# Optimization experiments

Measured on AMD Instinct MI355X. Metric: run time of the kernel, lower is better.

Reference implementation:

```python
import jax, jax.numpy as jnp
import numpy as np

INV_148 = 1.0 / 1.48  # scaling to align grids with flat-top gaussian


def _trilinear_sample(grid, pts):
    # grid: [C, D, H, W]; pts: [N, 3] in (x,y,z)=(W,H,D) normalized coords, align_corners=True,
    # padding_mode='zeros' (out-of-bounds corners contribute 0). Returns [C, N].
    C, D, H, W = grid.shape
    fx = (pts[:, 0] + 1.0) * 0.5 * (W - 1)
    fy = (pts[:, 1] + 1.0) * 0.5 * (H - 1)
    fz = (pts[:, 2] + 1.0) * 0.5 * (D - 1)
    x0 = jnp.floor(fx).astype(jnp.int32)
    y0 = jnp.floor(fy).astype(jnp.int32)
    z0 = jnp.floor(fz).astype(jnp.int32)
    wx, wy, wz = fx - x0, fy - y0, fz - z0
    out = jnp.zeros((C, pts.shape[0]), dtype=grid.dtype)
    for dz in (0, 1):
        for dy in (0, 1):
            for dx in (0, 1):
                xi, yi, zi = x0 + dx, y0 + dy, z0 + dz
                w = (wx if dx else 1.0 - wx) * (wy if dy else 1.0 - wy) * (wz if dz else 1.0 - wz)
                valid = ((xi >= 0) & (xi < W) & (yi >= 0) & (yi < H) & (zi >= 0) & (zi < D))
                v = grid[:, jnp.clip(zi, 0, D - 1), jnp.clip(yi, 0, H - 1), jnp.clip(xi, 0, W - 1)]
                out = out + v * (w * valid)
    return out


def setup_inputs() -> dict:
    key = jax.random.key(0)
    ks = jax.random.split(key, 10)
    G, Fch, Dg, N, NPL, OUT = 32, 2, 64, 524288, 64, 1
    in_dim = G * Fch
    x = jax.random.uniform(ks[0], (N, 3), minval=-1.0, maxval=1.0, dtype=jnp.float32)
    grid_scales = jax.random.uniform(ks[1], (G, 3), minval=1.5, maxval=2.5, dtype=jnp.float32)
    grid_translations = jax.random.uniform(ks[2], (G, 3), minval=-1.0, maxval=1.0, dtype=jnp.float32) * (grid_scales - 1.0)
    feature_grids = jax.random.uniform(ks[3], (G, Fch, Dg, Dg, Dg), minval=-0.001, maxval=0.001, dtype=jnp.float32)
    W0 = jax.random.normal(ks[4], (NPL, in_dim), dtype=jnp.float32) * (1.0 / np.sqrt(in_dim))
    b0 = jnp.zeros((NPL,), dtype=jnp.float32)
    W1 = jax.random.normal(ks[5], (NPL, NPL), dtype=jnp.float32) * (1.0 / np.sqrt(NPL))
    b1 = jnp.zeros((NPL,), dtype=jnp.float32)
    W2 = jax.random.normal(ks[6], (OUT, NPL), dtype=jnp.float32) * (1.0 / np.sqrt(NPL))
    b2 = jnp.zeros((OUT,), dtype=jnp.float32)
    return {"x": x, "grid_scales": grid_scales, "grid_translations": grid_translations,
            "feature_grids": feature_grids, "W0": W0, "b0": b0, "W1": W1, "b1": b1, "W2": W2, "b2": b2}


def reference(x, grid_scales, grid_translations, feature_grids, W0, b0, W1, b1, W2, b2):
    G = feature_grids.shape[0]
    N = x.shape[0]
    # transform(): per-grid affine (diag scale + translation), then * 1/1.48 -> [G, N, 3]
    local = (x[None, :, :] * grid_scales[:, None, :] + grid_translations[:, None, :]) * INV_148
    # forward detaches grid coords before grid_sample
    local = jax.lax.stop_gradient(local)
    feats = jax.vmap(_trilinear_sample)(feature_grids, local)  # [G, F, N]
    h = feats.reshape(G * feats.shape[1], N).T  # [N, G*F]
    h = jax.nn.relu(h @ W0.T + b0)
    h = jax.nn.relu(h @ W1.T + b1)
    return h @ W2.T + b2  # [N, n_outputs]
```

## Files before the change

kernel.cpp:

```cpp
#include <hip/hip_runtime.h>
#include <hip/hip_fp16.h>

#define NG    32
#define DG    64
#define NPL   64
#define CPD2  16
#define NC2   4096
#define NCELL 512
#define HPAD  4
#define BS    512
#define TV    4096
#define HS    68

typedef _Float16 half8 __attribute__((ext_vector_type(8)));
typedef float    floatx4 __attribute__((ext_vector_type(4)));

__global__ void pack_grids_kernel(const float* __restrict__ fg,
                                  uint4* __restrict__ pg, int total4) {
    int idx = blockIdx.x * blockDim.x + threadIdx.x;
    if (idx >= total4) return;
    int g  = idx >> 16;
    int v4 = (idx & 65535) << 2;
    const float* base = fg + ((size_t)g << 19);
    float4 a = *(const float4*)(base + v4);
    float4 b = *(const float4*)(base + (1 << 18) + v4);
    uint4 o;
    __half2 h;
    h = __floats2half2_rn(a.x, b.x); o.x = *(unsigned*)&h;
    h = __floats2half2_rn(a.y, b.y); o.y = *(unsigned*)&h;
    h = __floats2half2_rn(a.z, b.z); o.z = *(unsigned*)&h;
    h = __floats2half2_rn(a.w, b.w); o.w = *(unsigned*)&h;
    pg[idx] = o;
}

__device__ __forceinline__ int morton16(int cx, int cy, int cz) {
    int m = 0;
    #pragma unroll
    for (int b = 0; b < 4; ++b)
        m |= (((cx >> b) & 1) << (3 * b))
           | (((cy >> b) & 1) << (3 * b + 1))
           | (((cz >> b) & 1) << (3 * b + 2));
    return m;
}
__device__ __forceinline__ int cell_of(float px, float py, float pz) {
    int cx = min(max((int)((px + 1.0f) * (0.5f * CPD2)), 0), CPD2 - 1);
    int cy = min(max((int)((py + 1.0f) * (0.5f * CPD2)), 0), CPD2 - 1);
    int cz = min(max((int)((pz + 1.0f) * (0.5f * CPD2)), 0), CPD2 - 1);
    return morton16(cx, cy, cz);
}

__global__ __launch_bounds__(BS)
void hist_kernel(const float* __restrict__ x, int N, int* __restrict__ ghist) {
    __shared__ int lh[NC2];
    for (int i = threadIdx.x; i < NC2; i += BS) lh[i] = 0;
    __syncthreads();
    int n = blockIdx.x * BS + threadIdx.x;
    if (n < N) atomicAdd(&lh[cell_of(x[3*n], x[3*n+1], x[3*n+2])], 1);
    __syncthreads();
    for (int i = threadIdx.x; i < NC2; i += BS) {
        int c = lh[i];
        if (c) atomicAdd(&ghist[i * HPAD], c);
    }
}

__global__ __launch_bounds__(1024)
void scan_kernel(const int* __restrict__ ghist, int* __restrict__ gcursor,
                 int* __restrict__ cellstart) {
    __shared__ int tsum[1024];
    int t = threadIdx.x;
    int v0 = ghist[(t * 4 + 0) * HPAD];
    int v1 = ghist[(t * 4 + 1) * HPAD];
    int v2 = ghist[(t * 4 + 2) * HPAD];
    int v3 = ghist[(t * 4 + 3) * HPAD];
    tsum[t] = v0 + v1 + v2 + v3;
    __syncthreads();
    #pragma unroll
    for (int off = 1; off < 1024; off <<= 1) {
        int u = (t >= off) ? tsum[t - off] : 0;
        __syncthreads();
        tsum[t] += u;
        __syncthreads();
    }
    int base = (t == 0) ? 0 : tsum[t - 1];
    gcursor[(t*4+0)*HPAD] = base; cellstart[t*4+0] = base; base += v0;
    gcursor[(t*4+1)*HPAD] = base; cellstart[t*4+1] = base; base += v1;
    gcursor[(t*4+2)*HPAD] = base; cellstart[t*4+2] = base; base += v2;
    gcursor[(t*4+3)*HPAD] = base; cellstart[t*4+3] = base;
    if (t == 1023) cellstart[NC2] = tsum[1023];
}

__global__ __launch_bounds__(BS)
void scatter_kernel(const float* __restrict__ x, int N,
                    int* __restrict__ gcursor, float4* __restrict__ sorted,
                    int* __restrict__ nidx) {
    __shared__ int cnt[NC2];
    __shared__ int base[NC2];
    int tid = threadIdx.x;
    for (int i = tid; i < NC2; i += BS) cnt[i] = 0;
    __syncthreads();
    int n = blockIdx.x * BS + tid;
    float px = 0.f, py = 0.f, pz = 0.f;
    int c = 0, r = 0;
    bool act = (n < N);
    if (act) {
        px = x[3*n]; py = x[3*n+1]; pz = x[3*n+2];
        c = cell_of(px, py, pz);
        r = atomicAdd(&cnt[c], 1);
    }
    __syncthreads();
    for (int i = tid; i < NC2; i += BS) {
        int cc = cnt[i];
        base[i] = cc ? atomicAdd(&gcursor[i * HPAD], cc) : 0;
    }
    __syncthreads();
    if (act) {
        int pos = base[c] + r;
        sorted[pos] = make_float4(px, py, pz, 0.0f);
        nidx[pos]   = n;
    }
}

__device__ __forceinline__ float2 h2_to_f2(unsigned u) {
    __half2 h = *reinterpret_cast<__half2*>(&u);
    return __half22float2(h);
}

template<bool FAST>
__device__ __forceinline__ unsigned sample_tile(
    const unsigned* __restrict__ tl,
    float px, float py, float pz,
    float A0, float A1, float A2, float B0, float B1, float B2,
    int ox, int oy, int oz)
{
    float fx = fmaf(px, A0, B0);
    float fy = fmaf(py, A1, B1);
    float fz = fmaf(pz, A2, B2);
    float flx = floorf(fx), fly = floorf(fy), flz = floorf(fz);
    int x0 = (int)flx, y0 = (int)fly, z0 = (int)flz;
    float wx = fx - flx, wy = fy - fly, wz = fz - flz;

    float wxa0, wxa1, wya0, wya1, wza0, wza1;
    if (FAST) {
        wxa0 = 1.0f - wx; wxa1 = wx;
        wya0 = 1.0f - wy; wya1 = wy;
        wza0 = 1.0f - wz; wza1 = wz;
    } else {
        wxa0 = (x0 >= 0  && x0     < DG) ? (1.0f - wx) : 0.0f;
        wxa1 = (x0 >= -1 && x0 + 1 < DG) ? wx          : 0.0f;
        wya0 = (y0 >= 0  && y0     < DG) ? (1.0f - wy) : 0.0f;
        wya1 = (y0 >= -1 && y0 + 1 < DG) ? wy          : 0.0f;
        wza0 = (z0 >= 0  && z0     < DG) ? (1.0f - wz) : 0.0f;
        wza1 = (z0 >= -1 && z0 + 1 < DG) ? wz          : 0.0f;
    }
    int ix0 = min(max(x0     - ox, 0), 15);
    int ix1 = min(max(x0 + 1 - ox, 0), 15);
    int iy0 = (min(max(y0     - oy, 0), 15)) << 4;
    int iy1 = (min(max(y0 + 1 - oy, 0), 15)) << 4;
    int iz0 = (min(max(z0     - oz, 0), 15)) << 8;
    int iz1 = (min(max(z0 + 1 - oz, 0), 15)) << 8;

    float w00 = wya0 * wza0, w10 = wya1 * wza0;
    float w01 = wya0 * wza1, w11 = wya1 * wza1;

    float c0 = 0.0f, c1 = 0.0f;
    float2 v;
    v = h2_to_f2(tl[iz0+iy0+ix0]); c0 = fmaf(wxa0*w00, v.x, c0); c1 = fmaf(wxa0*w00, v.y, c1);
    v = h2_to_f2(tl[iz0+iy0+ix1]); c0 = fmaf(wxa1*w00, v.x, c0); c1 = fmaf(wxa1*w00, v.y, c1);
    v = h2_to_f2(tl[iz0+iy1+ix0]); c0 = fmaf(wxa0*w10, v.x, c0); c1 = fmaf(wxa0*w10, v.y, c1);
    v = h2_to_f2(tl[iz0+iy1+ix1]); c0 = fmaf(wxa1*w10, v.x, c0); c1 = fmaf(wxa1*w10, v.y, c1);
    v = h2_to_f2(tl[iz1+iy0+ix0]); c0 = fmaf(wxa0*w01, v.x, c0); c1 = fmaf(wxa0*w01, v.y, c1);
    v = h2_to_f2(tl[iz1+iy0+ix1]); c0 = fmaf(wxa1*w01, v.x, c0); c1 = fmaf(wxa1*w01, v.y, c1);
    v = h2_to_f2(tl[iz1+iy1+ix0]); c0 = fmaf(wxa0*w11, v.x, c0); c1 = fmaf(wxa0*w11, v.y, c1);
    v = h2_to_f2(tl[iz1+iy1+ix1]); c0 = fmaf(wxa1*w11, v.x, c0); c1 = fmaf(wxa1*w11, v.y, c1);

    __half2 hv = __floats2half2_rn(c0, c1);
    return *reinterpret_cast<unsigned*>(&hv);
}

__global__ __launch_bounds__(BS)
void gather_kernel(const float4* __restrict__ sorted,
                   const int*   __restrict__ cs16,
                   const float* __restrict__ scales,
                   const float* __restrict__ trans,
                   const unsigned* __restrict__ pg,
                   int4* __restrict__ featbuf, int N)
{
    __shared__ float    sA[NG * 3];
    __shared__ float    sB[NG * 3];
    __shared__ int      sO[NG * 3];
    __shared__ int      sCls[NG];
    __shared__ int      sList[NG + 1];
    __shared__ unsigned tile[2][TV];

    const int tid  = threadIdx.x;
    const int bid  = blockIdx.x;
    const int half = bid >> 9;
    const int cell = bid & 511;
    const int c    = ((cell & 7) << 6) + (cell >> 3);

    int s0c = cs16[c * 8];
    int ec  = cs16[c * 8 + 8];
    int cnt = ec - s0c;
    int hsz = (cnt + 1) >> 1;
    int start = s0c + half * hsz;
    int end   = min(ec, start + hsz);
    if (start >= end) return;

    int cx = (c & 1)        | (((c >> 3) & 1) << 1) | (((c >> 6) & 1) << 2);
    int cy = ((c >> 1) & 1) | (((c >> 4) & 1) << 1) | (((c >> 7) & 1) << 2);
    int cz = ((c >> 2) & 1) | (((c >> 5) & 1) << 1) | (((c >> 8) & 1) << 2);

    if (tid < NG * 3) {
        const float k = (1.0f / 1.48f) * 31.5f;
        float A  = scales[tid] * k;
        float Bv = trans[tid] * k + 31.5f;
        sA[tid] = A; sB[tid] = Bv;
        int d  = tid % 3;
        int cc = (d == 0) ? cx : ((d == 1) ? cy : cz);
        int o  = (int)floorf(fmaf((float)cc * 0.25f - 1.0f, A, Bv));
        sO[tid] = min(max(o, 0), 48);
    }
    __syncthreads();
    if (tid < NG) {
        bool skip = false, fast = true;
        #pragma unroll
        for (int d = 0; d < 3; ++d) {
            float A = sA[3 * tid + d], B = sB[3 * tid + d];
            int  cc = (d == 0) ? cx : ((d == 1) ? cy : cz);
            float lo = fmaf((float)cc, 0.25f, -1.0f) - 1e-4f;
            float hi = lo + 0.25f + 2e-4f;
            float fmn = fmaf(lo, A, B);
            float fmx = fmaf(hi, A, B);
            skip = skip || (fmx <= -1.0f) || (fmn >= 64.0f);
            fast = fast && (fmn >= 0.0f) && (fmx <= 63.0f);
        }
        sCls[tid] = skip ? 0 : (fast ? 1 : 2);
    }
    __syncthreads();
    if (tid == 0) {
        int n2 = 0;
        for (int g = 0; g < NG; ++g)
            if (sCls[g]) sList[n2++] = g;
        sList[NG] = n2;
    }
    __syncthreads();
    const int nAct = sList[NG];

    int  ip0 = start + tid,        ip1 = start + BS + tid;
    bool act0 = (ip0 < end),       act1 = (ip1 < end);
    float px0 = 0.f, py0 = 0.f, pz0 = 0.f;
    float px1 = 0.f, py1 = 0.f, pz1 = 0.f;
    if (act0) { float4 q = sorted[ip0]; px0 = q.x; py0 = q.y; pz0 = q.z; }
    if (act1) { float4 q = sorted[ip1]; px1 = q.x; py1 = q.y; pz1 = q.z; }

    if (nAct > 0) {
        int g0 = sList[0];
        int ox = sO[3*g0], oy = sO[3*g0+1], oz = sO[3*g0+2];
        const unsigned* gb = pg + ((size_t)g0 << 18);
        #pragma unroll
        for (int jj = 0; jj < 8; ++jj) {
            int v = tid + (jj << 9);
            tile[0][v] = gb[((oz + (v >> 8)) << 12) + ((oy + ((v >> 4) & 15)) << 6)
                            + ox + (v & 15)];
        }
    }
    __syncthreads();

    unsigned fp0[4], fp1[4];
    unsigned r[8];
    int j = 0;

    #pragma unroll 1
    for (int w = 0; w < 8; ++w) {
        #pragma unroll
        for (int q = 0; q < 4; ++q) {
            int g   = 4 * w + q;
            int cls = sCls[g];
            if (cls == 0) { fp0[q] = 0u; fp1[q] = 0u; continue; }

            const unsigned* tl = &tile[j & 1][0];
            bool more = (j + 1 < nAct);
            if (more) {
                int gn = sList[j + 1];
                int ox = sO[3*gn], oy = sO[3*gn+1], oz = sO[3*gn+2];
                const unsigned* gb = pg + ((size_t)gn << 18);
                #pragma unroll
                for (int jj = 0; jj < 8; ++jj) {
                    int v = tid + (jj << 9);
                    r[jj] = gb[((oz + (v >> 8)) << 12) + ((oy + ((v >> 4) & 15)) << 6)
                               + ox + (v & 15)];
                }
            }

            float A0 = sA[3*g], A1 = sA[3*g+1], A2 = sA[3*g+2];
            float B0 = sB[3*g], B1 = sB[3*g+1], B2 = sB[3*g+2];
            int   ox = sO[3*g], oy = sO[3*g+1], oz = sO[3*g+2];
            if (cls == 1) {
                fp0[q] = act0 ? sample_tile<true >(tl, px0,py0,pz0, A0,A1,A2,B0,B1,B2, ox,oy,oz) : 0u;
                fp1[q] = act1 ? sample_tile<true >(tl, px1,py1,pz1, A0,A1,A2,B0,B1,B2, ox,oy,oz) : 0u;
            } else {
                fp0[q] = act0 ? sample_tile<false>(tl, px0,py0,pz0, A0,A1,A2,B0,B1,B2, ox,oy,oz) : 0u;
                fp1[q] = act1 ? sample_tile<false>(tl, px1,py1,pz1, A0,A1,A2,B0,B1,B2, ox,oy,oz) : 0u;
            }

            if (more) {
                unsigned* td = &tile[(j & 1) ^ 1][0];
                #pragma unroll
                for (int jj = 0; jj < 8; ++jj) td[tid + (jj << 9)] = r[jj];
            }
            __syncthreads();
            ++j;
        }
        const size_t plane = (size_t)w * (size_t)N;
        if (act0) featbuf[plane + ip0] =
            make_int4((int)fp0[0], (int)fp0[1], (int)fp0[2], (int)fp0[3]);
        if (act1) featbuf[plane + ip1] =
            make_int4((int)fp1[0], (int)fp1[1], (int)fp1[2], (int)fp1[3]);
    }
}

#define MBS 256
__global__ __launch_bounds__(MBS)
void mlp_kernel(const int4* __restrict__ featbuf,
                const int* __restrict__ nidx,
                const float* __restrict__ W0, const float* __restrict__ b0,
                const float* __restrict__ W1, const float* __restrict__ b1,
                const float* __restrict__ W2, const float* __restrict__ b2,
                float* __restrict__ out, int N)
{
    __shared__ __align__(16) _Float16 sW0h[NPL * NPL];
    __shared__ __align__(16) _Float16 sW1h[NPL * NPL];
    __shared__ float sb0f[NPL], sb1f[NPL], sW2f[NPL];
    __shared__ __align__(16) _Float16 sH[4][NPL * HS];

    int tid = threadIdx.x;
    for (int i = tid; i < NPL * NPL; i += MBS) {
        sW0h[i] = (_Float16)W0[i];
        sW1h[i] = (_Float16)W1[i];
    }
    if (tid < NPL) { sb0f[tid] = b0[tid]; sb1f[tid] = b1[tid]; sW2f[tid] = W2[tid]; }
    __syncthreads();

    const int wave = tid >> 6;
    const int lane = tid & 63;
    const int l15  = lane & 15;
    const int kg   = lane >> 4;
    const long wbase = (long)blockIdx.x * MBS + wave * 64;
    if (wbase >= N) return;

    half8 B0[4][2], B1[4][2];
    float bias0[4], bias1[4], w2v[4];
    #pragma unroll
    for (int nt = 0; nt < 4; ++nt) {
        int ch = nt * 16 + l15;
        #pragma unroll
        for (int kh = 0; kh < 2; ++kh) {
            int k = kh * 32 + kg * 8;
            B0[nt][kh] = *(const half8*)&sW0h[ch * NPL + k];
            B1[nt][kh] = *(const half8*)&sW1h[ch * NPL + k];
        }
        bias0[nt] = sb0f[ch];
        bias1[nt] = sb1f[ch];
        w2v[nt]   = sW2f[ch];
    }

    _Float16* H = &sH[wave][0];

    floatx4 acc[4][4];
    #pragma unroll
    for (int mt = 0; mt < 4; ++mt) {
        long pt = wbase + mt * 16 + l15;
        if (pt > N - 1) pt = N - 1;
        int4 t0 = featbuf[(size_t)kg * N + pt];
        int4 t1 = featbuf[(size_t)(4 + kg) * N + pt];
        half8 a0 = *reinterpret_cast<half8*>(&t0);
        half8 a1 = *reinterpret_cast<half8*>(&t1);
        #pragma unroll
        for (int nt = 0; nt < 4; ++nt) {
            floatx4 cc = {0.f, 0.f, 0.f, 0.f};
            cc = __builtin_amdgcn_mfma_f32_16x16x32_f16(a0, B0[nt][0], cc, 0, 0, 0);
            cc = __builtin_amdgcn_mfma_f32_16x16x32_f16(a1, B0[nt][1], cc, 0, 0, 0);
            acc[mt][nt] = cc;
        }
    }
    #pragma unroll
    for (int mt = 0; mt < 4; ++mt)
        #pragma unroll
        for (int nt = 0; nt < 4; ++nt) {
            int ch = nt * 16 + l15;
            #pragma unroll
            for (int r = 0; r < 4; ++r) {
                float v = fmaxf(acc[mt][nt][r] + bias0[nt], 0.0f);
                H[(mt * 16 + kg * 4 + r) * HS + ch] = (_Float16)v;
            }
        }

    floatx4 acc2[4][4];
    #pragma unroll
    for (int mt = 0; mt < 4; ++mt) {
        const _Float16* hp = &H[(mt * 16 + l15) * HS];
        half8 a0 = *(const half8*)&hp[kg * 8];
        half8 a1 = *(const half8*)&hp[32 + kg * 8];
        #pragma unroll
        for (int nt = 0; nt < 4; ++nt) {
            floatx4 cc = {0.f, 0.f, 0.f, 0.f};
            cc = __builtin_amdgcn_mfma_f32_16x16x32_f16(a0, B1[nt][0], cc, 0, 0, 0);
            cc = __builtin_amdgcn_mfma_f32_16x16x32_f16(a1, B1[nt][1], cc, 0, 0, 0);
            acc2[mt][nt] = cc;
        }
    }

    float p[4][4];
    #pragma unroll
    for (int mt = 0; mt < 4; ++mt)
        #pragma unroll
        for (int r = 0; r < 4; ++r) p[mt][r] = 0.0f;
    #pragma unroll
    for (int mt = 0; mt < 4; ++mt)
        #pragma unroll
        for (int nt = 0; nt < 4; ++nt)
            #pragma unroll
            for (int r = 0; r < 4; ++r) {
                float v = fmaxf(acc2[mt][nt][r] + bias1[nt], 0.0f);
                p[mt][r] = fmaf(v, w2v[nt], p[mt][r]);
            }
    #pragma unroll
    for (int mt = 0; mt < 4; ++mt)
        #pragma unroll
        for (int r = 0; r < 4; ++r) {
            float s = p[mt][r];
            s += __shfl_xor(s, 1);
            s += __shfl_xor(s, 2);
            s += __shfl_xor(s, 4);
            s += __shfl_xor(s, 8);
            p[mt][r] = s;
        }

    float* HF = (float*)H;
    float ob = b2[0];
    if (l15 == 0) {
        #pragma unroll
        for (int mt = 0; mt < 4; ++mt)
            #pragma unroll
            for (int r = 0; r < 4; ++r)
                HF[mt * 16 + kg * 4 + r] = p[mt][r] + ob;
    }
    long pos = wbase + lane;
    if (pos < N) out[nidx[pos]] = HF[lane];
}

__global__ __launch_bounds__(256)
void fused_fallback_kernel(const float* __restrict__ x,
                           const float* __restrict__ scales,
                           const float* __restrict__ trans,
                           const __half2* __restrict__ pg,
                           const float* __restrict__ W0, const float* __restrict__ b0,
                           const float* __restrict__ W1, const float* __restrict__ b1,
                           const float* __restrict__ W2, const float* __restrict__ b2,
                           float* __restrict__ out, int N)
{
    __shared__ float sW0[NPL*NPL], sW1[NPL*NPL], sW2[NPL], sb0[NPL], sb1[NPL];
    __shared__ float sA[NG*3], sB[NG*3];
    const int tid = threadIdx.x;
    for (int i = tid; i < NPL*NPL; i += 256) { sW0[i] = W0[i]; sW1[i] = W1[i]; }
    if (tid < NPL) { sW2[tid] = W2[tid]; sb0[tid] = b0[tid]; sb1[tid] = b1[tid]; }
    if (tid < NG*3) {
        const float k = (1.0f / 1.48f) * 31.5f;
        sA[tid] = scales[tid] * k;
        sB[tid] = trans[tid] * k + 31.5f;
    }
    __syncthreads();
    int n = blockIdx.x * 256 + tid;
    if (n >= N) return;
    float px = x[3*n], py = x[3*n+1], pz = x[3*n+2];
    float feat[2*NG];
    #pragma unroll
    for (int g = 0; g < NG; ++g) {
        float fx = fmaf(px, sA[3*g+0], sB[3*g+0]);
        float fy = fmaf(py, sA[3*g+1], sB[3*g+1]);
        float fz = fmaf(pz, sA[3*g+2], sB[3*g+2]);
        float c0 = 0.f, c1 = 0.f;
        if (fx > -1.f && fx < 64.f && fy > -1.f && fy < 64.f && fz > -1.f && fz < 64.f) {
            float flx = floorf(fx), fly = floorf(fy), flz = floorf(fz);
            int x0 = (int)flx, y0 = (int)fly, z0 = (int)flz;
            float wx = fx-flx, wy = fy-fly, wz = fz-flz;
            float wxa[2], wya[2], wza[2]; int xia[2], yia[2], zia[2];
            wxa[0] = (x0 >= 0  && x0   < DG) ? (1.f-wx) : 0.f;
            wxa[1] = (x0 >= -1 && x0+1 < DG) ? wx : 0.f;
            wya[0] = (y0 >= 0  && y0   < DG) ? (1.f-wy) : 0.f;
            wya[1] = (y0 >= -1 && y0+1 < DG) ? wy : 0.f;
            wza[0] = (z0 >= 0  && z0   < DG) ? (1.f-wz) : 0.f;
            wza[1] = (z0 >= -1 && z0+1 < DG) ? wz : 0.f;
            xia[0] = min(max(x0,0),DG-1); xia[1] = min(max(x0+1,0),DG-1);
            yia[0] = min(max(y0,0),DG-1); yia[1] = min(max(y0+1,0),DG-1);
            zia[0] = min(max(z0,0),DG-1); zia[1] = min(max(z0+1,0),DG-1);
            #pragma unroll
            for (int dz = 0; dz < 2; ++dz)
                #pragma unroll
                for (int dy = 0; dy < 2; ++dy) {
                    int rowoff = (zia[dz] << 12) + (yia[dy] << 6);
                    float wyz = wya[dy] * wza[dz];
                    #pragma unroll
                    for (int dx = 0; dx < 2; ++dx) {
                        float w = wxa[dx] * wyz;
                        float2 vf = __half22float2(pg[(g << 18) + rowoff + xia[dx]]);
                        c0 = fmaf(w, vf.x, c0); c1 = fmaf(w, vf.y, c1);
                    }
                }
        }
        feat[2*g] = c0; feat[2*g+1] = c1;
    }
    float h1[NPL];
    #pragma unroll
    for (int j = 0; j < NPL; j += 2) {
        float a0=0.f,a1=0.f,a2=0.f,a3=0.f;
        const float* r0 = &sW0[j*NPL]; const float* r1 = &sW0[(j+1)*NPL];
        #pragma unroll
        for (int k = 0; k < NPL; k += 2) {
            a0 = fmaf(feat[k],r0[k],a0); a1 = fmaf(feat[k+1],r0[k+1],a1);
            a2 = fmaf(feat[k],r1[k],a2); a3 = fmaf(feat[k+1],r1[k+1],a3);
        }
        h1[j] = fmaxf((a0+a1)+sb0[j],0.f); h1[j+1] = fmaxf((a2+a3)+sb0[j+1],0.f);
    }
    #pragma unroll
    for (int j = 0; j < NPL; j += 2) {
        float a0=0.f,a1=0.f,a2=0.f,a3=0.f;
        const float* r0 = &sW1[j*NPL]; const float* r1 = &sW1[(j+1)*NPL];
        #pragma unroll
        for (int k = 0; k < NPL; k += 2) {
            a0 = fmaf(h1[k],r0[k],a0); a1 = fmaf(h1[k+1],r0[k+1],a1);
            a2 = fmaf(h1[k],r1[k],a2); a3 = fmaf(h1[k+1],r1[k+1],a3);
        }
        feat[j] = fmaxf((a0+a1)+sb1[j],0.f); feat[j+1] = fmaxf((a2+a3)+sb1[j+1],0.f);
    }
    float a0 = 0.f, a1 = 0.f;
    #pragma unroll
    for (int k = 0; k < NPL; k += 2) { a0 = fmaf(feat[k],sW2[k],a0); a1 = fmaf(feat[k+1],sW2[k+1],a1); }
    out[n] = (a0+a1) + b2[0];
}

extern "C" void kernel_launch(void* const* d_in, const int* in_sizes, int n_in,
                              void* d_out, int out_size, void* d_ws, size_t ws_size,
                              hipStream_t stream) {
    const float* x  = (const float*)d_in[0];
    const float* gs = (const float*)d_in[1];
    const float* gt = (const float*)d_in[2];
    const float* fg = (const float*)d_in[3];
    const float* W0 = (const float*)d_in[4];
    const float* b0 = (const float*)d_in[5];
    const float* W1 = (const float*)d_in[6];
    const float* b1 = (const float*)d_in[7];
    const float* W2 = (const float*)d_in[8];
    const float* b2 = (const float*)d_in[9];
    float* out = (float*)d_out;

    const int N = out_size;

    const size_t pg_bytes   = (size_t)NG * (1 << 18) * 4;
    const size_t feat_bytes = (size_t)N * 8 * sizeof(int4);
    const size_t sort_bytes = (size_t)N * sizeof(float4);
    const size_t nidx_bytes = (size_t)N * sizeof(int);
    const size_t cs_bytes   = ((NC2 + 1 + 15) & ~15) * sizeof(int);
    const size_t hist_bytes = (size_t)NC2 * HPAD * sizeof(int);
    const size_t need_full  = pg_bytes + feat_bytes + sort_bytes + nidx_bytes
                            + cs_bytes + 2 * hist_bytes;

    if (ws_size >= need_full) {
        char* w = (char*)d_ws;
        unsigned* pg        = (unsigned*)w;  w += pg_bytes;
        int4*     featbuf   = (int4*)w;      w += feat_bytes;
        float4*   sorted    = (float4*)w;    w += sort_bytes;
        int*      nidx      = (int*)w;       w += nidx_bytes;
        int*      cellstart = (int*)w;       w += cs_bytes;
        int*      ghist     = (int*)w;       w += hist_bytes;
        int*      gcur      = (int*)w;

        int total4 = NG << 16;
        int nblk   = (N + BS - 1) / BS;
        pack_grids_kernel<<<(total4 + 255) / 256, 256, 0, stream>>>(fg, (uint4*)pg, total4);
        hipMemsetAsync(ghist, 0, hist_bytes, stream);
        hist_kernel<<<nblk, BS, 0, stream>>>(x, N, ghist);
        scan_kernel<<<1, 1024, 0, stream>>>(ghist, gcur, cellstart);
        scatter_kernel<<<nblk, BS, 0, stream>>>(x, N, gcur, sorted, nidx);
        gather_kernel<<<NCELL * 2, BS, 0, stream>>>(
            sorted, cellstart, gs, gt, pg, featbuf, N);
        mlp_kernel<<<(N + MBS - 1) / MBS, MBS, 0, stream>>>(
            featbuf, nidx, W0, b0, W1, b1, W2, b2, out, N);
    } else if (ws_size >= pg_bytes) {
        unsigned* pg = (unsigned*)d_ws;
        int total4 = NG << 16;
        pack_grids_kernel<<<(total4 + 255) / 256, 256, 0, stream>>>(fg, (uint4*)pg, total4);
        fused_fallback_kernel<<<(N + 255) / 256, 256, 0, stream>>>(
            x, gs, gt, (const __half2*)pg, W0, b0, W1, b1, W2, b2, out, N);
    } else {
        fused_fallback_kernel<<<(N + 255) / 256, 256, 0, stream>>>(
            x, gs, gt, (const __half2*)fg, W0, b0, W1, b1, W2, b2, out, N);
    }
}
```

Measured before the change: 189.3 us.

## Use one 1024-thread block per cell with swizzled LDS tiles in gather

The gather kernel now launches one 1024-thread block per spatial cell instead of two 512-thread blocks splitting each cell. Each grid tile is therefore loaded into LDS once per cell rather than twice, halving the global tile traffic and the per-grid barrier work per point. The LDS tile is stored with an XOR swizzle on z-slices to reduce bank conflicts. The fast path also drops its index clamps, with the fast-class threshold tightened to keep indices in range. The cost is fewer blocks in flight (512) and a larger workgroup, which may reduce occupancy and load balance across cells of uneven size.

```diff
diff --git a/kernel.cpp b/kernel.cpp
--- a/kernel.cpp
+++ b/kernel.cpp
@@ -9,8 +9,11 @@
 #define NCELL 512
 #define HPAD  4
 #define BS    512
+#define GBS   1024
 #define TV    4096
 #define HS    68
+
+#define SWZ(i) ((i) ^ (((i) >> 6) & 28))
 
 typedef _Float16 half8 __attribute__((ext_vector_type(8)));
 typedef float    floatx4 __attribute__((ext_vector_type(4)));
@@ -140,10 +143,14 @@
     float wx = fx - flx, wy = fy - fly, wz = fz - flz;
 
     float wxa0, wxa1, wya0, wya1, wza0, wza1;
+    int ix0, ix1, iy0, iy1, iz0, iz1;
     if (FAST) {
         wxa0 = 1.0f - wx; wxa1 = wx;
         wya0 = 1.0f - wy; wya1 = wy;
         wza0 = 1.0f - wz; wza1 = wz;
+        ix0 = x0 - ox;            ix1 = ix0 + 1;
+        iy0 = (y0 - oy) << 4;     iy1 = iy0 + 16;
+        iz0 = (z0 - oz) << 8;     iz1 = iz0 + 256;
     } else {
         wxa0 = (x0 >= 0  && x0     < DG) ? (1.0f - wx) : 0.0f;
         wxa1 = (x0 >= -1 && x0 + 1 < DG) ? wx          : 0.0f;
@@ -151,33 +158,35 @@
         wya1 = (y0 >= -1 && y0 + 1 < DG) ? wy          : 0.0f;
         wza0 = (z0 >= 0  && z0     < DG) ? (1.0f - wz) : 0.0f;
         wza1 = (z0 >= -1 && z0 + 1 < DG) ? wz          : 0.0f;
-    }
-    int ix0 = min(max(x0     - ox, 0), 15);
-    int ix1 = min(max(x0 + 1 - ox, 0), 15);
-    int iy0 = (min(max(y0     - oy, 0), 15)) << 4;
-    int iy1 = (min(max(y0 + 1 - oy, 0), 15)) << 4;
-    int iz0 = (min(max(z0     - oz, 0), 15)) << 8;
-    int iz1 = (min(max(z0 + 1 - oz, 0), 15)) << 8;
+        ix0 = min(max(x0     - ox, 0), 15);
+        ix1 = min(max(x0 + 1 - ox, 0), 15);
+        iy0 = (min(max(y0     - oy, 0), 15)) << 4;
+        iy1 = (min(max(y0 + 1 - oy, 0), 15)) << 4;
+        iz0 = (min(max(z0     - oz, 0), 15)) << 8;
+        iz1 = (min(max(z0 + 1 - oz, 0), 15)) << 8;
+    }
+    const int m0 = (iz0 >> 6) & 28;
+    const int m1 = (iz1 >> 6) & 28;
 
     float w00 = wya0 * wza0, w10 = wya1 * wza0;
     float w01 = wya0 * wza1, w11 = wya1 * wza1;
 
     float c0 = 0.0f, c1 = 0.0f;
     float2 v;
-    v = h2_to_f2(tl[iz0+iy0+ix0]); c0 = fmaf(wxa0*w00, v.x, c0); c1 = fmaf(wxa0*w00, v.y, c1);
-    v = h2_to_f2(tl[iz0+iy0+ix1]); c0 = fmaf(wxa1*w00, v.x, c0); c1 = fmaf(wxa1*w00, v.y, c1);
-    v = h2_to_f2(tl[iz0+iy1+ix0]); c0 = fmaf(wxa0*w10, v.x, c0); c1 = fmaf(wxa0*w10, v.y, c1);
-    v = h2_to_f2(tl[iz0+iy1+ix1]); c0 = fmaf(wxa1*w10, v.x, c0); c1 = fmaf(wxa1*w10, v.y, c1);
-    v = h2_to_f2(tl[iz1+iy0+ix0]); c0 = fmaf(wxa0*w01, v.x, c0); c1 = fmaf(wxa0*w01, v.y, c1);
-    v = h2_to_f2(tl[iz1+iy0+ix1]); c0 = fmaf(wxa1*w01, v.x, c0); c1 = fmaf(wxa1*w01, v.y, c1);
-    v = h2_to_f2(tl[iz1+iy1+ix0]); c0 = fmaf(wxa0*w11, v.x, c0); c1 = fmaf(wxa0*w11, v.y, c1);
-    v = h2_to_f2(tl[iz1+iy1+ix1]); c0 = fmaf(wxa1*w11, v.x, c0); c1 = fmaf(wxa1*w11, v.y, c1);
+    v = h2_to_f2(tl[(iz0+iy0+ix0)^m0]); c0 = fmaf(wxa0*w00, v.x, c0); c1 = fmaf(wxa0*w00, v.y, c1);
+    v = h2_to_f2(tl[(iz0+iy0+ix1)^m0]); c0 = fmaf(wxa1*w00, v.x, c0); c1 = fmaf(wxa1*w00, v.y, c1);
+    v = h2_to_f2(tl[(iz0+iy1+ix0)^m0]); c0 = fmaf(wxa0*w10, v.x, c0); c1 = fmaf(wxa0*w10, v.y, c1);
+    v = h2_to_f2(tl[(iz0+iy1+ix1)^m0]); c0 = fmaf(wxa1*w10, v.x, c0); c1 = fmaf(wxa1*w10, v.y, c1);
+    v = h2_to_f2(tl[(iz1+iy0+ix0)^m1]); c0 = fmaf(wxa0*w01, v.x, c0); c1 = fmaf(wxa0*w01, v.y, c1);
+    v = h2_to_f2(tl[(iz1+iy0+ix1)^m1]); c0 = fmaf(wxa1*w01, v.x, c0); c1 = fmaf(wxa1*w01, v.y, c1);
+    v = h2_to_f2(tl[(iz1+iy1+ix0)^m1]); c0 = fmaf(wxa0*w11, v.x, c0); c1 = fmaf(wxa0*w11, v.y, c1);
+    v = h2_to_f2(tl[(iz1+iy1+ix1)^m1]); c0 = fmaf(wxa1*w11, v.x, c0); c1 = fmaf(wxa1*w11, v.y, c1);
 
     __half2 hv = __floats2half2_rn(c0, c1);
     return *reinterpret_cast<unsigned*>(&hv);
 }
 
-__global__ __launch_bounds__(BS)
+__global__ __launch_bounds__(GBS)
 void gather_kernel(const float4* __restrict__ sorted,
                    const int*   __restrict__ cs16,
                    const float* __restrict__ scales,
@@ -193,18 +202,12 @@
     __shared__ unsigned tile[2][TV];
 
     const int tid  = threadIdx.x;
-    const int bid  = blockIdx.x;
-    const int half = bid >> 9;
-    const int cell = bid & 511;
+    const int cell = blockIdx.x;
     const int c    = ((cell & 7) << 6) + (cell >> 3);
 
     int s0c = cs16[c * 8];
     int ec  = cs16[c * 8 + 8];
-    int cnt = ec - s0c;
-    int hsz = (cnt + 1) >> 1;
-    int start = s0c + half * hsz;
-    int end   = min(ec, start + hsz);
-    if (start >= end) return;
+    if (s0c >= ec) return;
 
     int cx = (c & 1)        | (((c >> 3) & 1) << 1) | (((c >> 6) & 1) << 2);
     int cy = ((c >> 1) & 1) | (((c >> 4) & 1) << 1) | (((c >> 7) & 1) << 2);
@@ -232,7 +235,7 @@
             float fmn = fmaf(lo, A, B);
             float fmx = fmaf(hi, A, B);
             skip = skip || (fmx <= -1.0f) || (fmn >= 64.0f);
-            fast = fast && (fmn >= 0.0f) && (fmx <= 63.0f);
+            fast = fast && (fmn >= 0.0f) && (fmx <= 62.9f);
         }
         sCls[tid] = skip ? 0 : (fast ? 1 : 2);
     }
@@ -246,8 +249,8 @@
     __syncthreads();
     const int nAct = sList[NG];
 
-    int  ip0 = start + tid,        ip1 = start + BS + tid;
-    bool act0 = (ip0 < end),       act1 = (ip1 < end);
+    int  ip0 = s0c + tid,        ip1 = s0c + GBS + tid;
+    bool act0 = (ip0 < ec),      act1 = (ip1 < ec);
     float px0 = 0.f, py0 = 0.f, pz0 = 0.f;
     float px1 = 0.f, py1 = 0.f, pz1 = 0.f;
     if (act0) { float4 q = sorted[ip0]; px0 = q.x; py0 = q.y; pz0 = q.z; }
@@ -258,16 +261,16 @@
         int ox = sO[3*g0], oy = sO[3*g0+1], oz = sO[3*g0+2];
         const unsigned* gb = pg + ((size_t)g0 << 18);
         #pragma unroll
-        for (int jj = 0; jj < 8; ++jj) {
-            int v = tid + (jj << 9);
-            tile[0][v] = gb[((oz + (v >> 8)) << 12) + ((oy + ((v >> 4) & 15)) << 6)
-                            + ox + (v & 15)];
+        for (int jj = 0; jj < 4; ++jj) {
+            int v = tid + (jj << 10);
+            tile[0][SWZ(v)] = gb[((oz + (v >> 8)) << 12) + ((oy + ((v >> 4) & 15)) << 6)
+                                 + ox + (v & 15)];
         }
     }
     __syncthreads();
 
     unsigned fp0[4], fp1[4];
-    unsigned r[8];
+    unsigned r[4];
     int j = 0;
 
     #pragma unroll 1
@@ -285,8 +288,8 @@
                 int ox = sO[3*gn], oy = sO[3*gn+1], oz = sO[3*gn+2];
                 const unsigned* gb = pg + ((size_t)gn << 18);
                 #pragma unroll
-                for (int jj = 0; jj < 8; ++jj) {
-                    int v = tid + (jj << 9);
+                for (int jj = 0; jj < 4; ++jj) {
+                    int v = tid + (jj << 10);
                     r[jj] = gb[((oz + (v >> 8)) << 12) + ((oy + ((v >> 4) & 15)) << 6)
                                + ox + (v & 15)];
                 }
@@ -295,18 +298,24 @@
             float A0 = sA[3*g], A1 = sA[3*g+1], A2 = sA[3*g+2];
             float B0 = sB[3*g], B1 = sB[3*g+1], B2 = sB[3*g+2];
             int   ox = sO[3*g], oy = sO[3*g+1], oz = sO[3*g+2];
+            fp1[q] = 0u;
             if (cls == 1) {
                 fp0[q] = act0 ? sample_tile<true >(tl, px0,py0,pz0, A0,A1,A2,B0,B1,B2, ox,oy,oz) : 0u;
-                fp1[q] = act1 ? sample_tile<true >(tl, px1,py1,pz1, A0,A1,A2,B0,B1,B2, ox,oy,oz) : 0u;
+                if (act1)
+                    fp1[q] = sample_tile<true >(tl, px1,py1,pz1, A0,A1,A2,B0,B1,B2, ox,oy,oz);
             } else {
                 fp0[q] = act0 ? sample_tile<false>(tl, px0,py0,pz0, A0,A1,A2,B0,B1,B2, ox,oy,oz) : 0u;
-                fp1[q] = act1 ? sample_tile<false>(tl, px1,py1,pz1, A0,A1,A2,B0,B1,B2, ox,oy,oz) : 0u;
+                if (act1)
+                    fp1[q] = sample_tile<false>(tl, px1,py1,pz1, A0,A1,A2,B0,B1,B2, ox,oy,oz);
             }
 
             if (more) {
                 unsigned* td = &tile[(j & 1) ^ 1][0];
                 #pragma unroll
-                for (int jj = 0; jj < 8; ++jj) td[tid + (jj << 9)] = r[jj];
+                for (int jj = 0; jj < 4; ++jj) {
+                    int v = tid + (jj << 10);
+                    td[SWZ(v)] = r[jj];
+                }
             }
             __syncthreads();
             ++j;
@@ -582,7 +591,7 @@
         hist_kernel<<<nblk, BS, 0, stream>>>(x, N, ghist);
         scan_kernel<<<1, 1024, 0, stream>>>(ghist, gcur, cellstart);
         scatter_kernel<<<nblk, BS, 0, stream>>>(x, N, gcur, sorted, nidx);
-        gather_kernel<<<NCELL * 2, BS, 0, stream>>>(
+        gather_kernel<<<NCELL, GBS, 0, stream>>>(
             sorted, cellstart, gs, gt, pg, featbuf, N);
         mlp_kernel<<<(N + MBS - 1) / MBS, MBS, 0, stream>>>(
             featbuf, nidx, W0, b0, W1, b1, W2, b2, out, N);
```

After: 186.4 us. No clear change (-1.5%).
